# Performance work log

Measured on AMD Instinct MI355X. Metric: run time of the kernel, lower is better.

Reference implementation:

```python
import jax, jax.numpy as jnp
import numpy as np

H = 768
NH = 12
HD = H // NH  # 64


def setup_inputs() -> dict:
    key = jax.random.key(0)
    ks = jax.random.split(key, 10)
    B, S = 8, 1024
    x = jax.random.normal(ks[0], (B, S, H), dtype=jnp.float32)
    attention_mask = jax.random.randint(ks[1], (B, S), 0, 2, dtype=jnp.int32)
    s = 1.0 / np.sqrt(H)
    Wq = jax.random.normal(ks[2], (H, H), jnp.float32) * s
    bq = jnp.zeros((H,), jnp.float32)
    Wk = jax.random.normal(ks[3], (H, H), jnp.float32) * s
    bk = jnp.zeros((H,), jnp.float32)
    Wv = jax.random.normal(ks[4], (H, H), jnp.float32) * s
    bv = jnp.zeros((H,), jnp.float32)
    Wo = jax.random.normal(ks[5], (H, H), jnp.float32) * s
    bo = jnp.zeros((H,), jnp.float32)
    return {"x": x, "attention_mask": attention_mask,
            "Wq": Wq, "bq": bq, "Wk": Wk, "bk": bk,
            "Wv": Wv, "bv": bv, "Wo": Wo, "bo": bo}


def reference(x, attention_mask, Wq, bq, Wk, bk, Wv, bv, Wo, bo):
    B, S, _ = x.shape
    scale = HD ** -0.5
    # projections -> [B, NH, S, HD]
    def split_heads(t):
        return t.reshape(B, S, NH, HD).transpose(0, 2, 1, 3)
    q = split_heads(x @ Wq.T + bq)
    k = split_heads(x @ Wk.T + bk)
    v = split_heads(x @ Wv.T + bv)
    scores = jnp.einsum('bhqd,bhkd->bhqk', q, k) * scale  # [B,NH,S,S]
    mask = attention_mask[:, None, None, :]  # [B,1,1,S]
    scores = jnp.where(mask == 0, jnp.float32(-10000.0), scores)
    probs = jax.nn.softmax(scores, axis=-1)
    ctx = jnp.einsum('bhqk,bhkd->bhqd', probs, v)  # [B,NH,S,HD]
    ctx = ctx.transpose(0, 2, 1, 3).reshape(B, S, H)
    out = ctx @ Wo.T + bo
    return out
```

## Files before the change

kernel.cpp:

```cpp
#include <hip/hip_runtime.h>
#include <hip/hip_bf16.h>

#define HDIM 768
#define NH 12
#define HD 64
#define BB 8
#define SS 1024
#define MROWS (BB*SS)
#define NQKV (3*HDIM)

#define SCL2E 0.18033688011f
#define MASKNEG -14426.9504f

typedef __attribute__((ext_vector_type(8))) short bf16x8;
typedef __attribute__((ext_vector_type(4))) float f32x4;

__device__ __forceinline__ unsigned short f2bf(float f) {
    unsigned int u = __float_as_uint(f);
    unsigned int r = (u + 0x7fffu + ((u >> 16) & 1u)) >> 16;
    return (unsigned short)r;
}

__device__ __forceinline__ void gload_lds16(const void* gsrc, void* ldst) {
    __builtin_amdgcn_global_load_lds(
        (const __attribute__((address_space(1))) unsigned int*)gsrc,
        (__attribute__((address_space(3))) unsigned int*)ldst,
        16, 0, 0);
}

__global__ void pack_all(const float* __restrict__ x,
                         const float* __restrict__ Wq, const float* __restrict__ Wk,
                         const float* __restrict__ Wv, const float* __restrict__ Wo,
                         const float* __restrict__ bq, const float* __restrict__ bk,
                         const float* __restrict__ bv, const int* __restrict__ m,
                         unsigned short* __restrict__ xb, unsigned short* __restrict__ wqkv,
                         unsigned short* __restrict__ wo,
                         float* __restrict__ biasq, float* __restrict__ madd)
{
    const int tid = blockIdx.x * blockDim.x + threadIdx.x;
    const int stride = gridDim.x * blockDim.x;
    for (int i = tid; i < 2162688; i += stride) {
        const float* src; unsigned short* dst; int off;
        if (i < 1572864) { src = x; dst = xb; off = i; }
        else {
            int j = i - 1572864;
            int seg = j / 147456;
            off = j - seg * 147456;
            src = (seg == 0) ? Wq : (seg == 1) ? Wk : (seg == 2) ? Wv : Wo;
            dst = (seg == 3) ? wo : wqkv + seg * (HDIM * HDIM);
        }
        float4 v = reinterpret_cast<const float4*>(src)[off];
        union { unsigned short u[4]; unsigned long long q; } o;
        o.u[0] = f2bf(v.x); o.u[1] = f2bf(v.y); o.u[2] = f2bf(v.z); o.u[3] = f2bf(v.w);
        reinterpret_cast<unsigned long long*>(dst)[off] = o.q;
    }
    if (tid < 3 * HDIM)
        biasq[tid] = (tid < HDIM) ? bq[tid] : (tid < 2 * HDIM) ? bk[tid - HDIM] : bv[tid - 2 * HDIM];
    if (tid < BB * SS)
        madd[tid] = (m[tid] == 0) ? MASKNEG : 0.0f;
}

template<int MODE>
__global__ __launch_bounds__(256)
void gemm_bt(const unsigned short* __restrict__ A,
             const unsigned short* __restrict__ Bw,
             const float* __restrict__ bias,
             unsigned short* __restrict__ qb,
             unsigned short* __restrict__ kb,
             unsigned short* __restrict__ vtb,
             float* __restrict__ fout,
             int K, int gridN)
{
    __shared__ unsigned short As[2][128 * 64];
    __shared__ unsigned short Bs[2][128 * 64];
    const int tid  = threadIdx.x;
    const int wave = tid >> 6;
    const int lane = tid & 63;

    const int nwg = gridDim.x;
    const int cpx = nwg >> 3;
    const int wg  = (blockIdx.x & 7) * cpx + (blockIdx.x >> 3);
    const int bm = (wg / gridN) * 128;
    const int bn = (wg % gridN) * 128;

    const int wm = (wave >> 1) * 64;
    const int wn = (wave & 1) * 64;
    const int lr  = lane & 15;
    const int hv  = lane >> 4;
    const int e3  = lr & 7;
    const int srow = lane >> 3;
    const int sg   = lane & 7;

    f32x4 zero4 = {0.f, 0.f, 0.f, 0.f};
    f32x4 acc[4][4];
#pragma unroll
    for (int i = 0; i < 4; i++)
#pragma unroll
        for (int j = 0; j < 4; j++) acc[i][j] = zero4;

    auto stage = [&](int buf, int k0) {
        const int gk = (sg ^ srow) * 8;
#pragma unroll
        for (int jj = 0; jj < 4; ++jj) {
            int i = wave * 4 + jj;
            gload_lds16(A  + (size_t)(bm + i * 8 + srow) * K + k0 + gk, &As[buf][i * 8 * 64]);
            gload_lds16(Bw + (size_t)(bn + i * 8 + srow) * K + k0 + gk, &Bs[buf][i * 8 * 64]);
        }
    };

    stage(0, 0);
    if (K > 64) stage(1, 64);

    int buf = 0;
    for (int k0 = 0; k0 < K; k0 += 64) {
        if (k0 + 64 < K) { asm volatile("s_waitcnt vmcnt(8)" ::: "memory"); }
        else             { asm volatile("s_waitcnt vmcnt(0)" ::: "memory"); }
        __builtin_amdgcn_s_barrier();
        __builtin_amdgcn_sched_barrier(0);

        bf16x8 af[4][2], bf[4][2];
#pragma unroll
        for (int mi = 0; mi < 4; mi++)
#pragma unroll
            for (int kk = 0; kk < 2; kk++)
                af[mi][kk] = *(const bf16x8*)
                    &As[buf][(wm + mi * 16 + lr) * 64 + ((kk * 4 + hv) ^ e3) * 8];
#pragma unroll
        for (int ni = 0; ni < 4; ni++)
#pragma unroll
            for (int kk = 0; kk < 2; kk++)
                bf[ni][kk] = *(const bf16x8*)
                    &Bs[buf][(wn + ni * 16 + lr) * 64 + ((kk * 4 + hv) ^ e3) * 8];

#pragma unroll
        for (int kk = 0; kk < 2; kk++)
#pragma unroll
            for (int mi = 0; mi < 4; mi++)
#pragma unroll
                for (int ni = 0; ni < 4; ni++)
                    acc[mi][ni] = __builtin_amdgcn_mfma_f32_16x16x32_bf16(
                        af[mi][kk], bf[ni][kk], acc[mi][ni], 0, 0, 0);

        __builtin_amdgcn_s_barrier();
        if (k0 + 128 < K) stage(buf, k0 + 128);
        buf ^= 1;
    }

    const int rgrp = lane >> 4;
#pragma unroll
    for (int mi = 0; mi < 4; mi++)
#pragma unroll
        for (int ni = 0; ni < 4; ni++)
#pragma unroll
            for (int r = 0; r < 4; r++) {
                int m = bm + wm + mi * 16 + rgrp * 4 + r;
                int n = bn + wn + ni * 16 + lr;
                float v = acc[mi][ni][r] + bias[n];
                if (MODE == 0) {
                    int which = n / HDIM;
                    int nn = n - which * HDIM;
                    int h = nn >> 6, d = nn & 63;
                    int b = m >> 10, s = m & 1023;
                    unsigned short bvv = f2bf(v);
                    if (which == 0)      qb [(((size_t)(b * NH + h)) * SS + s) * HD + d] = bvv;
                    else if (which == 1) kb [(((size_t)(b * NH + h)) * SS + s) * HD + d] = bvv;
                    else                 vtb[(((size_t)(b * NH + h)) * HD + d) * SS + s] = bvv;
                } else {
                    fout[(size_t)m * HDIM + n] = v;
                }
            }
}

__global__ __launch_bounds__(256, 4)
void attn_kernel(const unsigned short* __restrict__ qb,
                 const unsigned short* __restrict__ kb,
                 const unsigned short* __restrict__ vtb,
                 const float* __restrict__ maskadd,
                 unsigned short* __restrict__ ctx)
{
    __shared__ unsigned short Ks[64][64];
    __shared__ unsigned short Vs[64][64];
    __shared__ unsigned short Ps[4][16][64];

    const int tid  = threadIdx.x;
    const int wave = tid >> 6;
    const int lane = tid & 63;
    const int wg = (blockIdx.x & 7) * 192 + (blockIdx.x >> 3);
    const int qt = wg & 15;
    const int h  = (wg >> 4) % NH;
    const int b  = wg / 192;
    const int bh = b * NH + h;
    const int q0 = qt * 64 + wave * 16;
    const int lr  = lane & 15;
    const int hi  = lane >> 4;
    const int e3  = lr & 7;
    const int srow = lane >> 3;
    const int sg   = lane & 7;

    const unsigned short* Qp = qb  + (size_t)bh * SS * HD;
    const unsigned short* Kp = kb  + (size_t)bh * SS * HD;
    const unsigned short* Vp = vtb + (size_t)bh * HD * SS;
    const float* madd = maskadd + b * SS;

    bf16x8 aq[2];
#pragma unroll
    for (int kk = 0; kk < 2; kk++)
        aq[kk] = *(const bf16x8*)&Qp[(size_t)(q0 + lr) * HD + kk * 32 + hi * 8];

    f32x4 zero4 = {0.f, 0.f, 0.f, 0.f};
    f32x4 o[4];
#pragma unroll
    for (int i = 0; i < 4; i++) o[i] = zero4;
    float plsum = 0.f;

    bf16x8 kreg[2], vreg[2];
    auto ld = [&](int t0) {
#pragma unroll
        for (int jj = 0; jj < 2; ++jj) {
            int rr = (wave * 2 + jj) * 8 + srow;
            kreg[jj] = *(const bf16x8*)&Kp[(size_t)(t0 + rr) * HD + sg * 8];
            vreg[jj] = *(const bf16x8*)&Vp[(size_t)rr * SS + t0 + sg * 8];
        }
    };
    auto wr = [&]() {
        const int slot = (sg ^ srow) * 8;
#pragma unroll
        for (int jj = 0; jj < 2; ++jj) {
            int rr = (wave * 2 + jj) * 8 + srow;
            *(bf16x8*)&Ks[rr][slot] = kreg[jj];
            *(bf16x8*)&Vs[rr][slot] = vreg[jj];
        }
    };

    ld(0);
    wr();
    __syncthreads();

    for (int t0 = 0; t0 < SS; t0 += 64) {
        const bool more = (t0 + 64 < SS);
        if (more) ld(t0 + 64);

        f32x4 sacc[4];
#pragma unroll
        for (int ni = 0; ni < 4; ni++) sacc[ni] = zero4;
        __builtin_amdgcn_s_setprio(1);
#pragma unroll
        for (int kk = 0; kk < 2; kk++)
#pragma unroll
            for (int ni = 0; ni < 4; ni++) {
                bf16x8 kf = *(const bf16x8*)&Ks[ni * 16 + lr][((kk * 4 + hi) ^ e3) * 8];
                sacc[ni] = __builtin_amdgcn_mfma_f32_16x16x32_bf16(kf, aq[kk], sacc[ni], 0, 0, 0);
            }
        __builtin_amdgcn_s_setprio(0);

        float4 md[4];
#pragma unroll
        for (int ni = 0; ni < 4; ni++)
            md[ni] = *(const float4*)&madd[t0 + ni * 16 + hi * 4];

        float p[4][4];
#pragma unroll
        for (int ni = 0; ni < 4; ni++) {
            p[ni][0] = __builtin_amdgcn_exp2f(fmaf(sacc[ni][0], SCL2E, md[ni].x));
            p[ni][1] = __builtin_amdgcn_exp2f(fmaf(sacc[ni][1], SCL2E, md[ni].y));
            p[ni][2] = __builtin_amdgcn_exp2f(fmaf(sacc[ni][2], SCL2E, md[ni].z));
            p[ni][3] = __builtin_amdgcn_exp2f(fmaf(sacc[ni][3], SCL2E, md[ni].w));
            plsum += p[ni][0] + p[ni][1] + p[ni][2] + p[ni][3];
        }

#pragma unroll
        for (int ni = 0; ni < 4; ni++) {
            union { __hip_bfloat162 h2[2]; unsigned long long q; } u;
            u.h2[0] = __float22bfloat162_rn(make_float2(p[ni][0], p[ni][1]));
            u.h2[1] = __float22bfloat162_rn(make_float2(p[ni][2], p[ni][3]));
            *(unsigned long long*)&Ps[wave][lr][((4 * ni + hi) ^ (e3 << 1)) * 4] = u.q;
        }

        __builtin_amdgcn_s_setprio(1);
#pragma unroll
        for (int ks = 0; ks < 2; ks++) {
            bf16x8 pa = *(const bf16x8*)&Ps[wave][lr][((8 * ks + 2 * hi) ^ (e3 << 1)) * 4];
#pragma unroll
            for (int nd = 0; nd < 4; nd++) {
                bf16x8 vb = *(const bf16x8*)&Vs[nd * 16 + lr][((4 * ks + hi) ^ e3) * 8];
                o[nd] = __builtin_amdgcn_mfma_f32_16x16x32_bf16(pa, vb, o[nd], 0, 0, 0);
            }
        }
        __builtin_amdgcn_s_setprio(0);

        __syncthreads();
        if (more) {
            wr();
            __syncthreads();
        }
    }

    float lrun = plsum;
    lrun += __shfl_xor(lrun, 16);
    lrun += __shfl_xor(lrun, 32);
    float iv[4];
#pragma unroll
    for (int r = 0; r < 4; r++) iv[r] = 1.0f / __shfl(lrun, hi * 4 + r, 16);
#pragma unroll
    for (int r = 0; r < 4; r++) {
        int grow = b * SS + qt * 64 + wave * 16 + hi * 4 + r;
#pragma unroll
        for (int nd = 0; nd < 4; nd++)
            ctx[(size_t)grow * HDIM + h * HD + nd * 16 + lr] = f2bf(o[nd][r] * iv[r]);
    }
}

extern "C" void kernel_launch(void* const* d_in, const int* in_sizes, int n_in,
                              void* d_out, int out_size, void* d_ws, size_t ws_size,
                              hipStream_t stream)
{
    const float* x    = (const float*)d_in[0];
    const int*   amask= (const int*)d_in[1];
    const float* Wq   = (const float*)d_in[2];
    const float* bq   = (const float*)d_in[3];
    const float* Wk   = (const float*)d_in[4];
    const float* bk   = (const float*)d_in[5];
    const float* Wv   = (const float*)d_in[6];
    const float* bv   = (const float*)d_in[7];
    const float* Wo   = (const float*)d_in[8];
    const float* bo   = (const float*)d_in[9];
    float* out = (float*)d_out;

    char* ws = (char*)d_ws;
    unsigned short* xb   = (unsigned short*)(ws);
    unsigned short* wqkv = (unsigned short*)(ws + 12582912);
    unsigned short* wo   = (unsigned short*)(ws + 16121856);
    float*          biasq= (float*)(ws + 17301504);
    unsigned short* qb   = (unsigned short*)(ws + 17310720);
    unsigned short* kb   = (unsigned short*)(ws + 29893632);
    unsigned short* vtb  = (unsigned short*)(ws + 42476544);
    unsigned short* ctx  = (unsigned short*)(ws + 55059456);
    float*          madd = (float*)(ws + 67642368);

    pack_all<<<2048, 256, 0, stream>>>(x, Wq, Wk, Wv, Wo, bq, bk, bv, amask,
                                       xb, wqkv, wo, biasq, madd);

    gemm_bt<0><<<(MROWS / 128) * (NQKV / 128), 256, 0, stream>>>(
        xb, wqkv, biasq, qb, kb, vtb, nullptr, HDIM, NQKV / 128);

    attn_kernel<<<(SS / 64) * NH * BB, 256, 0, stream>>>(qb, kb, vtb, madd, ctx);

    gemm_bt<1><<<(MROWS / 128) * (HDIM / 128), 256, 0, stream>>>(
        ctx, wo, bo, nullptr, nullptr, nullptr, out, HDIM, HDIM / 128);
}
```

Before: 139.7 us.

## Double per-wave query rows in attention to reuse K/V tiles

Each attention workgroup now processes 128 query rows (32 per wave, as two 16-row groups) instead of 64, so every K/V tile staged in shared memory and every K/V fragment read from LDS feeds twice as many MFMAs. The grid is halved and the block-to-(batch, head, tile) mapping is adjusted to match. This cuts redundant global loads of K/V and the LDS traffic per unit of work. In exchange it raises register pressure from doubled accumulators and query fragments, and the smaller grid of 768 blocks may reduce occupancy and latency hiding.

Result: slower. 159.6 us (+14.3%).

```diff
diff --git a/kernel.cpp b/kernel.cpp
--- a/kernel.cpp
+++ b/kernel.cpp
@@ -180,17 +180,17 @@
 {
     __shared__ unsigned short Ks[64][64];
     __shared__ unsigned short Vs[64][64];
-    __shared__ unsigned short Ps[4][16][64];
+    __shared__ unsigned short Ps[4][32][64];
 
     const int tid  = threadIdx.x;
     const int wave = tid >> 6;
     const int lane = tid & 63;
-    const int wg = (blockIdx.x & 7) * 192 + (blockIdx.x >> 3);
-    const int qt = wg & 15;
-    const int h  = (wg >> 4) % NH;
-    const int b  = wg / 192;
+    const int wg = (blockIdx.x & 7) * 96 + (blockIdx.x >> 3);
+    const int qt = wg & 7;
+    const int h  = (wg >> 3) % NH;
+    const int b  = wg / 96;
     const int bh = b * NH + h;
-    const int q0 = qt * 64 + wave * 16;
+    const int q0 = qt * 128 + wave * 32;
     const int lr  = lane & 15;
     const int hi  = lane >> 4;
     const int e3  = lr & 7;
@@ -202,16 +202,20 @@
     const unsigned short* Vp = vtb + (size_t)bh * HD * SS;
     const float* madd = maskadd + b * SS;
 
-    bf16x8 aq[2];
-#pragma unroll
-    for (int kk = 0; kk < 2; kk++)
-        aq[kk] = *(const bf16x8*)&Qp[(size_t)(q0 + lr) * HD + kk * 32 + hi * 8];
+    bf16x8 aq[2][2];
+#pragma unroll
+    for (int g = 0; g < 2; g++)
+#pragma unroll
+        for (int kk = 0; kk < 2; kk++)
+            aq[g][kk] = *(const bf16x8*)&Qp[(size_t)(q0 + g * 16 + lr) * HD + kk * 32 + hi * 8];
 
     f32x4 zero4 = {0.f, 0.f, 0.f, 0.f};
-    f32x4 o[4];
-#pragma unroll
-    for (int i = 0; i < 4; i++) o[i] = zero4;
-    float plsum = 0.f;
+    f32x4 o[2][4];
+#pragma unroll
+    for (int g = 0; g < 2; g++)
+#pragma unroll
+        for (int i = 0; i < 4; i++) o[g][i] = zero4;
+    float plsum0 = 0.f, plsum1 = 0.f;
 
     bf16x8 kreg[2], vreg[2];
     auto ld = [&](int t0) {
@@ -240,16 +244,19 @@
         const bool more = (t0 + 64 < SS);
         if (more) ld(t0 + 64);
 
-        f32x4 sacc[4];
-#pragma unroll
-        for (int ni = 0; ni < 4; ni++) sacc[ni] = zero4;
+        f32x4 sacc[2][4];
+#pragma unroll
+        for (int g = 0; g < 2; g++)
+#pragma unroll
+            for (int ni = 0; ni < 4; ni++) sacc[g][ni] = zero4;
         __builtin_amdgcn_s_setprio(1);
 #pragma unroll
         for (int kk = 0; kk < 2; kk++)
 #pragma unroll
             for (int ni = 0; ni < 4; ni++) {
                 bf16x8 kf = *(const bf16x8*)&Ks[ni * 16 + lr][((kk * 4 + hi) ^ e3) * 8];
-                sacc[ni] = __builtin_amdgcn_mfma_f32_16x16x32_bf16(kf, aq[kk], sacc[ni], 0, 0, 0);
+                sacc[0][ni] = __builtin_amdgcn_mfma_f32_16x16x32_bf16(kf, aq[0][kk], sacc[0][ni], 0, 0, 0);
+                sacc[1][ni] = __builtin_amdgcn_mfma_f32_16x16x32_bf16(kf, aq[1][kk], sacc[1][ni], 0, 0, 0);
             }
         __builtin_amdgcn_s_setprio(0);
 
@@ -258,32 +265,41 @@
         for (int ni = 0; ni < 4; ni++)
             md[ni] = *(const float4*)&madd[t0 + ni * 16 + hi * 4];
 
-        float p[4][4];
 #pragma unroll
         for (int ni = 0; ni < 4; ni++) {
-            p[ni][0] = __builtin_amdgcn_exp2f(fmaf(sacc[ni][0], SCL2E, md[ni].x));
-            p[ni][1] = __builtin_amdgcn_exp2f(fmaf(sacc[ni][1], SCL2E, md[ni].y));
-            p[ni][2] = __builtin_amdgcn_exp2f(fmaf(sacc[ni][2], SCL2E, md[ni].z));
-            p[ni][3] = __builtin_amdgcn_exp2f(fmaf(sacc[ni][3], SCL2E, md[ni].w));
-            plsum += p[ni][0] + p[ni][1] + p[ni][2] + p[ni][3];
-        }
-
+            float p0 = __builtin_amdgcn_exp2f(fmaf(sacc[0][ni][0], SCL2E, md[ni].x));
+            float p1 = __builtin_amdgcn_exp2f(fmaf(sacc[0][ni][1], SCL2E, md[ni].y));
+            float p2 = __builtin_amdgcn_exp2f(fmaf(sacc[0][ni][2], SCL2E, md[ni].z));
+            float p3 = __builtin_amdgcn_exp2f(fmaf(sacc[0][ni][3], SCL2E, md[ni].w));
+            plsum0 += p0 + p1 + p2 + p3;
+            union { __hip_bfloat162 h2[2]; unsigned long long q; } u;
+            u.h2[0] = __float22bfloat162_rn(make_float2(p0, p1));
+            u.h2[1] = __float22bfloat162_rn(make_float2(p2, p3));
+            *(unsigned long long*)&Ps[wave][lr][((4 * ni + hi) ^ (e3 << 1)) * 4] = u.q;
+        }
 #pragma unroll
         for (int ni = 0; ni < 4; ni++) {
+            float p0 = __builtin_amdgcn_exp2f(fmaf(sacc[1][ni][0], SCL2E, md[ni].x));
+            float p1 = __builtin_amdgcn_exp2f(fmaf(sacc[1][ni][1], SCL2E, md[ni].y));
+            float p2 = __builtin_amdgcn_exp2f(fmaf(sacc[1][ni][2], SCL2E, md[ni].z));
+            float p3 = __builtin_amdgcn_exp2f(fmaf(sacc[1][ni][3], SCL2E, md[ni].w));
+            plsum1 += p0 + p1 + p2 + p3;
             union { __hip_bfloat162 h2[2]; unsigned long long q; } u;
-            u.h2[0] = __float22bfloat162_rn(make_float2(p[ni][0], p[ni][1]));
-            u.h2[1] = __float22bfloat162_rn(make_float2(p[ni][2], p[ni][3]));
-            *(unsigned long long*)&Ps[wave][lr][((4 * ni + hi) ^ (e3 << 1)) * 4] = u.q;
+            u.h2[0] = __float22bfloat162_rn(make_float2(p0, p1));
+            u.h2[1] = __float22bfloat162_rn(make_float2(p2, p3));
+            *(unsigned long long*)&Ps[wave][16 + lr][((4 * ni + hi) ^ (e3 << 1)) * 4] = u.q;
         }
 
         __builtin_amdgcn_s_setprio(1);
 #pragma unroll
         for (int ks = 0; ks < 2; ks++) {
-            bf16x8 pa = *(const bf16x8*)&Ps[wave][lr][((8 * ks + 2 * hi) ^ (e3 << 1)) * 4];
+            bf16x8 pa0 = *(const bf16x8*)&Ps[wave][lr]     [((8 * ks + 2 * hi) ^ (e3 << 1)) * 4];
+            bf16x8 pa1 = *(const bf16x8*)&Ps[wave][16 + lr][((8 * ks + 2 * hi) ^ (e3 << 1)) * 4];
 #pragma unroll
             for (int nd = 0; nd < 4; nd++) {
                 bf16x8 vb = *(const bf16x8*)&Vs[nd * 16 + lr][((4 * ks + hi) ^ e3) * 8];
-                o[nd] = __builtin_amdgcn_mfma_f32_16x16x32_bf16(pa, vb, o[nd], 0, 0, 0);
+                o[0][nd] = __builtin_amdgcn_mfma_f32_16x16x32_bf16(pa0, vb, o[0][nd], 0, 0, 0);
+                o[1][nd] = __builtin_amdgcn_mfma_f32_16x16x32_bf16(pa1, vb, o[1][nd], 0, 0, 0);
             }
         }
         __builtin_amdgcn_s_setprio(0);
@@ -295,18 +311,22 @@
         }
     }
 
-    float lrun = plsum;
-    lrun += __shfl_xor(lrun, 16);
-    lrun += __shfl_xor(lrun, 32);
-    float iv[4];
-#pragma unroll
-    for (int r = 0; r < 4; r++) iv[r] = 1.0f / __shfl(lrun, hi * 4 + r, 16);
-#pragma unroll
-    for (int r = 0; r < 4; r++) {
-        int grow = b * SS + qt * 64 + wave * 16 + hi * 4 + r;
-#pragma unroll
-        for (int nd = 0; nd < 4; nd++)
-            ctx[(size_t)grow * HDIM + h * HD + nd * 16 + lr] = f2bf(o[nd][r] * iv[r]);
+#pragma unroll
+    for (int g = 0; g < 2; g++) {
+        float lrun = (g == 0) ? plsum0 : plsum1;
+        lrun += __shfl_xor(lrun, 16);
+        lrun += __shfl_xor(lrun, 32);
+        float iv[4];
+#pragma unroll
+        for (int r = 0; r < 4; r++) iv[r] = 1.0f / __shfl(lrun, hi * 4 + r, 16);
+#pragma unroll
+        for (int r = 0; r < 4; r++) {
+            int grow = b * SS + q0 + g * 16 + hi * 4 + r;
+#pragma unroll
+            for (int nd = 0; nd < 4; nd++)
+                ctx[(size_t)grow * HDIM + h * HD + nd * 16 + lr] =
+                    f2bf(((g == 0) ? o[0][nd][r] : o[1][nd][r]) * iv[r]);
+        }
     }
 }
 
@@ -343,7 +363,7 @@
     gemm_bt<0><<<(MROWS / 128) * (NQKV / 128), 256, 0, stream>>>(
         xb, wqkv, biasq, qb, kb, vtb, nullptr, HDIM, NQKV / 128);
 
-    attn_kernel<<<(SS / 64) * NH * BB, 256, 0, stream>>>(qb, kb, vtb, madd, ctx);
+    attn_kernel<<<(SS / 128) * NH * BB, 256, 0, stream>>>(qb, kb, vtb, madd, ctx);
 
     gemm_bt<1><<<(MROWS / 128) * (HDIM / 128), 256, 0, stream>>>(
         ctx, wo, bo, nullptr, nullptr, nullptr, out, HDIM, HDIM / 128);
```
